# Kernel tuning notes

Measured on AMD Instinct MI355X. Metric: run time of the kernel, lower is better.

The kernel has to match this reference:

```python
import jax, jax.numpy as jnp
import numpy as np
from jax import lax

EPS = 1e-6  # LayerNorm2d eps


def _ln2d(x, w, b):
    # channel-wise LayerNorm over dim 1 of [B,C,H,W]
    mu = jnp.mean(x, axis=1, keepdims=True)
    var = jnp.mean((x - mu) ** 2, axis=1, keepdims=True)
    return (x - mu) / jnp.sqrt(var + EPS) * w[None, :, None, None] + b[None, :, None, None]


def _conv1x1(x, w, b):
    # w: [O, C]
    return jnp.einsum('bchw,oc->bohw', x, w) + b[None, :, None, None]


def _dconv(x, w, b):
    # 3x3 conv, dilation 4, padding 4 -> same H,W. w: [O, C, 3, 3]
    y = lax.conv_general_dilated(x, w, window_strides=(1, 1),
                                 padding=((4, 4), (4, 4)), rhs_dilation=(4, 4),
                                 dimension_numbers=('NCHW', 'OIHW', 'NCHW'))
    return y + b[None, :, None, None]


def _forward(x_l, x_r, nl_w, nl_b, nr_w, nr_b, lp1_w, lp1_b, rp1_w, rp1_b,
             dl_w, dl_b, dr_w, dr_b, lp2_w, lp2_b, rp2_w, rp2_b, beta, gamma):
    c = x_l.shape[1]
    scale = c ** (-0.5)
    N_l = _ln2d(x_l, nl_w, nl_b)
    N_r = _ln2d(x_r, nr_w, nr_b)
    V_l = jnp.transpose(_conv1x1(x_l, lp2_w, lp2_b), (0, 2, 3, 1))   # [B,H,W,C]
    V_r = jnp.transpose(_conv1x1(x_r, rp2_w, rp2_b), (0, 2, 3, 1))
    Q_l = jnp.transpose(_conv1x1(N_l, lp1_w, lp1_b), (0, 2, 3, 1))   # [B,H,W,C]
    Q_r = jnp.transpose(_conv1x1(N_r, rp1_w, rp1_b), (0, 2, 3, 1))
    K_l_T = jnp.transpose(_dconv(N_l, dl_w, dl_b), (0, 2, 1, 3))     # [B,H,C,W]
    K_r_T = jnp.transpose(_dconv(N_r, dr_w, dr_b), (0, 2, 1, 3))
    # per-row cross attention: [B,H,W,W]
    attn_r2l = jnp.einsum('bhwc,bhcv->bhwv', Q_l, K_r_T) * scale
    attn_l2r = jnp.einsum('bhwc,bhcv->bhwv', Q_r, K_l_T) * scale
    F_r2l = jnp.einsum('bhwv,bhvc->bhwc', jax.nn.softmax(attn_r2l, axis=-1), V_r)
    F_l2r = jnp.einsum('bhwv,bhvc->bhwc', jax.nn.softmax(attn_l2r, axis=-1), V_l)
    F_r2l = jnp.transpose(F_r2l, (0, 3, 1, 2)) * beta   # [B,C,H,W]
    F_l2r = jnp.transpose(F_l2r, (0, 3, 1, 2)) * gamma
    return x_l + F_r2l, x_r + F_l2r


def setup_inputs() -> dict:
    key = jax.random.key(0)
    ks = jax.random.split(key, 12)
    B, C, H, W = 2, 128, 192, 512
    s = 0.02
    rn = lambda k, shp: s * jax.random.normal(k, shp, jnp.float32)
    return {
        'x_l': jax.random.normal(ks[0], (B, C, H, W), jnp.float32),
        'x_r': jax.random.normal(ks[1], (B, C, H, W), jnp.float32),
        'nl_w': jnp.ones((C,), jnp.float32), 'nl_b': jnp.zeros((C,), jnp.float32),
        'nr_w': jnp.ones((C,), jnp.float32), 'nr_b': jnp.zeros((C,), jnp.float32),
        'lp1_w': rn(ks[2], (C, C)), 'lp1_b': jnp.zeros((C,), jnp.float32),
        'rp1_w': rn(ks[3], (C, C)), 'rp1_b': jnp.zeros((C,), jnp.float32),
        'dl_w': rn(ks[4], (C, C, 3, 3)), 'dl_b': jnp.zeros((C,), jnp.float32),
        'dr_w': rn(ks[5], (C, C, 3, 3)), 'dr_b': jnp.zeros((C,), jnp.float32),
        'lp2_w': rn(ks[6], (C, C)), 'lp2_b': jnp.zeros((C,), jnp.float32),
        'rp2_w': rn(ks[7], (C, C)), 'rp2_b': jnp.zeros((C,), jnp.float32),
        'beta': 0.1 * jax.random.normal(ks[8], (1, C, 1, 1), jnp.float32),
        'gamma': 0.1 * jax.random.normal(ks[9], (1, C, 1, 1), jnp.float32),
    }


def reference(x_l, x_r, nl_w, nl_b, nr_w, nr_b, lp1_w, lp1_b, rp1_w, rp1_b,
              dl_w, dl_b, dr_w, dr_b, lp2_w, lp2_b, rp2_w, rp2_b, beta, gamma):
    return _forward(x_l, x_r, nl_w, nl_b, nr_w, nr_b, lp1_w, lp1_b, rp1_w, rp1_b,
                    dl_w, dl_b, dr_w, dr_b, lp2_w, lp2_b, rp2_w, rp2_b, beta, gamma)
```

## Files before the change

kernel.cpp:

```cpp
#include <hip/hip_runtime.h>
#include <stdint.h>

#define CC 128
#define HH 192
#define WW 512
#define BB 2
#define HW (HH*WW)
#define CHW (CC*HW)
#define TENS (BB*CHW)

typedef __attribute__((ext_vector_type(8))) short bf16x8;
typedef __attribute__((ext_vector_type(4))) float f32x4;
typedef __attribute__((ext_vector_type(4))) unsigned short u16x4;

__device__ __forceinline__ unsigned short f2bf(float f) {
    union { float f; unsigned u; } v; v.f = f;
    return (unsigned short)((v.u + 0x7FFFu + ((v.u >> 16) & 1u)) >> 16);
}
__device__ __forceinline__ float bf2f(unsigned short u) {
    union { unsigned u; float f; } v; v.u = ((unsigned)u) << 16;
    return v.f;
}
__device__ __forceinline__ uint32_t cvtpk(float lo, float hi) {
    uint32_t r;
    asm("v_cvt_pk_bf16_f32 %0, %1, %2" : "=v"(r) : "v"(lo), "v"(hi));
    return r;
}
__device__ __forceinline__ f32x4 MFMA(bf16x8 a, bf16x8 b, f32x4 c) {
    return __builtin_amdgcn_mfma_f32_16x16x32_bf16(a, b, c, 0, 0, 0);
}

__global__ __launch_bounds__(256) void wcast_k(
    const float* __restrict__ dlw, const float* __restrict__ drw,
    unsigned short* __restrict__ wd)
{
    int i = blockIdx.x * 256 + threadIdx.x;
    if (i >= 2 * 9 * CC * CC) return;
    int e  = i & 7;
    int l  = (i >> 3) & 63;
    int n_ = (i >> 9) & 3;
    int kk = (i >> 11) & 3;
    int oh = (i >> 13) & 1;
    int rest = i >> 14;
    int tap = rest % 9;
    int side = rest / 9;
    int o = oh * 64 + n_ * 16 + (l & 15);
    int c = kk * 32 + (l >> 4) * 8 + e;
    const float* src = side ? drw : dlw;
    wd[i] = f2bf(src[((size_t)o * CC + c) * 9 + tap]);
}

__global__ __launch_bounds__(256) void lnv_k(
    const float* __restrict__ xl, const float* __restrict__ xr,
    const float* __restrict__ nlw, const float* __restrict__ nlb,
    const float* __restrict__ nrw, const float* __restrict__ nrb,
    const float* __restrict__ wlp, const float* __restrict__ blp,
    const float* __restrict__ wrp, const float* __restrict__ brp,
    unsigned short* __restrict__ ntl, unsigned short* __restrict__ ntr,
    unsigned short* __restrict__ vlo, unsigned short* __restrict__ vro)
{
    const int side = blockIdx.y;
    const float* x  = side ? xr : xl;
    const float* nw = side ? nrw : nlw;
    const float* nb = side ? nrb : nlb;
    const float* wv = side ? wrp : wlp;
    const float* bv = side ? brp : blp;
    unsigned short* nt = side ? ntr : ntl;
    unsigned short* vo = side ? vro : vlo;
    const int bid = blockIdx.x;
    const int wt = bid & 7, h = (bid >> 3) % HH, b = bid / (8 * HH);
    const int w0 = wt * 64;
    const int t = threadIdx.x;

    __shared__ unsigned short sA[64][136];
    __shared__ unsigned short sB[128][136];
    __shared__ float red[8][64];
    __shared__ float smu[64], srs[64];

    {
        const int w = t & 63, cg = t >> 6;
        const float* xp = x + (size_t)b * CHW + (size_t)h * WW + w0 + w;
        float s = 0.f, q = 0.f;
        for (int i = 0; i < 16; i++) {
            int c = cg * 32 + i * 2;
            float v0 = xp[(size_t)c * HW];
            float v1 = xp[(size_t)(c + 1) * HW];
            *(uint32_t*)&sA[w][c] = cvtpk(v0, v1);
            s += v0 + v1; q += v0 * v0 + v1 * v1;
        }
        red[cg][w] = s; red[4 + cg][w] = q;
    }
    for (int it = 0; it < 16; it++) {
        int f = it * 1024 + t * 4;
        int o = f >> 7, c = f & 127;
        float4 v = *(const float4*)(wv + o * CC + c);
        *(uint32_t*)&sB[o][c]     = cvtpk(v.x, v.y);
        *(uint32_t*)&sB[o][c + 2] = cvtpk(v.z, v.w);
    }
    __syncthreads();
    if (t < 64) {
        float S = red[0][t] + red[1][t] + red[2][t] + red[3][t];
        float Q = red[4][t] + red[5][t] + red[6][t] + red[7][t];
        float mu = S * (1.f / CC);
        float var = fmaxf(Q * (1.f / CC) - mu * mu, 0.f);
        smu[t] = mu; srs[t] = rsqrtf(var + 1e-6f);
    }
    __syncthreads();
    {
        const int w = t >> 2, c0 = (t & 3) * 32;
        const float mu = smu[w], rs = srs[w];
        unsigned short* np = nt + ((size_t)(b * HH + h) * WW + w0 + w) * CC;
        for (int i = 0; i < 32; i += 2) {
            int c = c0 + i;
            float v0 = (bf2f(sA[w][c]) - mu) * rs * nw[c] + nb[c];
            float v1 = (bf2f(sA[w][c + 1]) - mu) * rs * nw[c + 1] + nb[c + 1];
            *(uint32_t*)&np[c] = cvtpk(v0, v1);
        }
    }
    const int wid = t >> 6, l = t & 63, lr = l & 15, lg = l >> 4;
    f32x4 acc[8] = {};
    for (int kk = 0; kk < 4; kk++) {
        bf16x8 a = *(const bf16x8*)&sA[wid * 16 + lr][kk * 32 + lg * 8];
#pragma unroll
        for (int n_ = 0; n_ < 8; n_++) {
            bf16x8 bb = *(const bf16x8*)&sB[n_ * 16 + lr][kk * 32 + lg * 8];
            acc[n_] = MFMA(a, bb, acc[n_]);
        }
    }
    unsigned short* vp = vo + ((size_t)(b * HH + h) * CC) * WW + w0;
    for (int n_ = 0; n_ < 8; n_++) {
        int o = n_ * 16 + lr;
        float bias = bv[o];
        uint2 uu;
        uu.x = cvtpk(acc[n_][0] + bias, acc[n_][1] + bias);
        uu.y = cvtpk(acc[n_][2] + bias, acc[n_][3] + bias);
        *(uint2*)&vp[(size_t)o * WW + wid * 16 + lg * 4] = uu;
    }
}

__global__ __launch_bounds__(256) void dconv_k(
    const unsigned short* __restrict__ ntl, const unsigned short* __restrict__ ntr,
    const unsigned short* __restrict__ wfr,
    const float* __restrict__ dlb, const float* __restrict__ drb,
    unsigned short* __restrict__ klo, unsigned short* __restrict__ kro)
{
    const int side = blockIdx.y;
    const unsigned short* nt = side ? ntr : ntl;
    const unsigned short* wbase = wfr + (size_t)side * 9 * 16384;
    const float* bd = side ? drb : dlb;
    unsigned short* ko = side ? kro : klo;
    const int bid0 = blockIdx.x;
    const int lgc = (bid0 & 7) * 192 + (bid0 >> 3);
    const int wt = lgc & 3;
    const int hb = lgc >> 2;
    const int h = hb % HH, b = hb / HH;
    const int w0 = wt * 128;
    const int t = threadIdx.x;
    const int wid = t >> 6, l = t & 63, lr = l & 15, lg = l >> 4;
    const int whalf = wid & 1, ohalf = wid >> 1;

    __shared__ unsigned short sA[136][136];

    f32x4 acc[4][4] = {};
    for (int dy = 0; dy < 3; dy++) {
        const int hh = h + 4 * (dy - 1);
        const bool hok = (hh >= 0 && hh < HH);
        __syncthreads();
        for (int f = t * 8; f < 136 * 128; f += 2048) {
            int wloc = f >> 7, c = f & 127;
            int w = w0 - 4 + wloc;
            bf16x8 v = {0, 0, 0, 0, 0, 0, 0, 0};
            if (hok && w >= 0 && w < WW)
                v = *(const bf16x8*)(nt + ((size_t)(b * HH + hh) * WW + w) * CC + c);
            *(bf16x8*)&sA[wloc][c] = v;
        }
        __syncthreads();
#pragma unroll
        for (int dx = 0; dx < 3; dx++) {
            const unsigned short* wtap =
                wbase + (size_t)(dy * 3 + dx) * 16384 + ohalf * 8192 + l * 8;
#pragma unroll
            for (int kk = 0; kk < 4; kk++) {
                bf16x8 bfr[4];
#pragma unroll
                for (int n_ = 0; n_ < 4; n_++)
                    bfr[n_] = *(const bf16x8*)(wtap + (kk * 4 + n_) * 512);
                bf16x8 af[4];
#pragma unroll
                for (int g = 0; g < 4; g++)
                    af[g] = *(const bf16x8*)&sA[whalf * 64 + g * 16 + lr + 4 * dx][kk * 32 + lg * 8];
#pragma unroll
                for (int g = 0; g < 4; g++)
#pragma unroll
                    for (int n_ = 0; n_ < 4; n_++)
                        acc[g][n_] = MFMA(af[g], bfr[n_], acc[g][n_]);
            }
        }
    }
    unsigned short* kp = ko + ((size_t)(b * HH + h) * WW + w0) * CC;
    for (int g = 0; g < 4; g++)
        for (int n_ = 0; n_ < 4; n_++) {
            int o = ohalf * 64 + n_ * 16 + lr;
            float bias = bd[o];
            for (int j = 0; j < 4; j++) {
                int w = whalf * 64 + g * 16 + lg * 4 + j;
                kp[(size_t)w * CC + o] = f2bf(acc[g][n_][j] + bias);
            }
        }
}

__global__ __launch_bounds__(256, 2) void attn_k(
    const unsigned short* __restrict__ ntl, const unsigned short* __restrict__ ntr,
    const unsigned short* __restrict__ kl,  const unsigned short* __restrict__ kr,
    const unsigned short* __restrict__ vtl, const unsigned short* __restrict__ vtr,
    const float* __restrict__ lp1w, const float* __restrict__ lp1b,
    const float* __restrict__ rp1w, const float* __restrict__ rp1b,
    const float* __restrict__ xl, const float* __restrict__ xr,
    const float* __restrict__ beta, const float* __restrict__ gamma,
    float* __restrict__ out)
{
    __shared__ __align__(16) char smem[52224];
    unsigned short* sQ  = (unsigned short*)smem;
    unsigned short* sWh = (unsigned short*)(smem + 34816);
    unsigned short* sKt = (unsigned short*)smem;
    unsigned short* sVt = (unsigned short*)(smem + 17408);

    const int dir = blockIdx.z;
    const unsigned short* nq  = dir ? ntr : ntl;
    const unsigned short* kws = dir ? kl : kr;
    const unsigned short* vws = dir ? vtl : vtr;
    const float* wq   = dir ? rp1w : lp1w;
    const float* bq   = dir ? rp1b : lp1b;
    const float* xres = dir ? xr : xl;
    const float* mult = dir ? gamma : beta;
    float* op = out + (size_t)dir * TENS;

    const int bid = blockIdx.x;
    const int xcd = bid & 7;
    const int s   = bid >> 3;
    const int qb  = s & 3;
    const int bh  = xcd + 8 * (s >> 2);
    const int q0  = qb * 128;
    const int t = threadIdx.x;
    const int wid = t >> 6, l = t & 63, lr = l & 15, lg = l >> 4;

    const unsigned short* ksrc = kws + (size_t)bh * WW * CC;
    const unsigned short* vsrc = vws + (size_t)bh * CC * WW;

    bf16x8 kreg[4], vreg[4];
#pragma unroll
    for (int it = 0; it < 4; it++) {
        int f = it * 2048 + t * 8;
        kreg[it] = *(const bf16x8*)(ksrc + f);
    }
#pragma unroll
    for (int it = 0; it < 4; it++) {
        int f = it * 2048 + t * 8;
        int c = f >> 6, k = f & 63;
        vreg[it] = *(const bf16x8*)(vsrc + (size_t)c * WW + k);
    }

    {
        const unsigned short* nsrc = nq + ((size_t)bh * WW + q0) * CC;
        for (int it = 0; it < 8; it++) {
            int f = it * 2048 + t * 8;
            *(bf16x8*)&sQ[(f >> 7) * 136 + (f & 127)] = *(const bf16x8*)(nsrc + f);
        }
        for (int it = 0; it < 8; it++) {
            int f = it * 1024 + t * 4;
            int o = f >> 7, c = f & 127;
            float4 v = *(const float4*)(wq + o * CC + c);
            *(uint32_t*)&sWh[o * 136 + c]     = cvtpk(v.x, v.y);
            *(uint32_t*)&sWh[o * 136 + c + 2] = cvtpk(v.z, v.w);
        }
    }
    f32x4 qacc[2][8] = {};
    __syncthreads();
    for (int kk = 0; kk < 4; kk++) {
        bf16x8 a0 = *(const bf16x8*)&sQ[(wid * 32 + lr) * 136 + kk * 32 + lg * 8];
        bf16x8 a1 = *(const bf16x8*)&sQ[(wid * 32 + 16 + lr) * 136 + kk * 32 + lg * 8];
#pragma unroll
        for (int n_ = 0; n_ < 4; n_++) {
            bf16x8 b = *(const bf16x8*)&sWh[(n_ * 16 + lr) * 136 + kk * 32 + lg * 8];
            qacc[0][n_] = MFMA(a0, b, qacc[0][n_]);
            qacc[1][n_] = MFMA(a1, b, qacc[1][n_]);
        }
    }
    __syncthreads();
    for (int it = 0; it < 8; it++) {
        int f = it * 1024 + t * 4;
        int o = f >> 7, c = f & 127;
        float4 v = *(const float4*)(wq + (o + 64) * CC + c);
        *(uint32_t*)&sWh[o * 136 + c]     = cvtpk(v.x, v.y);
        *(uint32_t*)&sWh[o * 136 + c + 2] = cvtpk(v.z, v.w);
    }
    __syncthreads();
    for (int kk = 0; kk < 4; kk++) {
        bf16x8 a0 = *(const bf16x8*)&sQ[(wid * 32 + lr) * 136 + kk * 32 + lg * 8];
        bf16x8 a1 = *(const bf16x8*)&sQ[(wid * 32 + 16 + lr) * 136 + kk * 32 + lg * 8];
#pragma unroll
        for (int n_ = 0; n_ < 4; n_++) {
            bf16x8 b = *(const bf16x8*)&sWh[(n_ * 16 + lr) * 136 + kk * 32 + lg * 8];
            qacc[0][4 + n_] = MFMA(a0, b, qacc[0][4 + n_]);
            qacc[1][4 + n_] = MFMA(a1, b, qacc[1][4 + n_]);
        }
    }
    __syncthreads();
    {
        const float SCL = 0.08838834764831845f * 1.4426950408889634f;
#pragma unroll
        for (int mg = 0; mg < 2; mg++)
#pragma unroll
            for (int n_ = 0; n_ < 8; n_++) {
                float bias = bq[n_ * 16 + lr];
#pragma unroll
                for (int j = 0; j < 4; j++)
                    sQ[(wid * 32 + mg * 16 + lg * 4 + j) * 136 + n_ * 16 + lr] =
                        f2bf((qacc[mg][n_][j] + bias) * SCL);
            }
    }
    __syncthreads();
    bf16x8 qf[2][4];
#pragma unroll
    for (int qg = 0; qg < 2; qg++)
#pragma unroll
        for (int kk = 0; kk < 4; kk++)
            qf[qg][kk] = *(const bf16x8*)&sQ[(wid * 32 + qg * 16 + lr) * 136 + kk * 32 + lg * 8];

    f32x4 oacc[8][2] = {};
    float mrow[2] = {-1e30f, -1e30f};
    float lrow[2] = {0.f, 0.f};
    const int src0 = lr + ((l & 16) << 1);
    const int src1 = src0 + 16;
    const int hi = lg >> 1;

    for (int kb = 0; kb < 8; kb++) {
        __syncthreads();
#pragma unroll
        for (int it = 0; it < 4; it++) {
            int f = it * 2048 + t * 8;
            *(bf16x8*)&sKt[(f >> 7) * 136 + (f & 127)] = kreg[it];
        }
#pragma unroll
        for (int it = 0; it < 4; it++) {
            int f = it * 2048 + t * 8;
            int c = f >> 6, k = f & 63;
            *(bf16x8*)&sVt[c * 72 + k] = vreg[it];
        }
        if (kb < 7) {
#pragma unroll
            for (int it = 0; it < 4; it++) {
                int f = it * 2048 + t * 8;
                kreg[it] = *(const bf16x8*)(ksrc + (kb + 1) * 64 * CC + f);
            }
#pragma unroll
            for (int it = 0; it < 4; it++) {
                int f = it * 2048 + t * 8;
                int c = f >> 6, k = f & 63;
                vreg[it] = *(const bf16x8*)(vsrc + (size_t)c * WW + (kb + 1) * 64 + k);
            }
        }
        __syncthreads();
        f32x4 sacc[2][4] = {};
        __builtin_amdgcn_s_setprio(1);
        for (int kk = 0; kk < 4; kk++)
#pragma unroll
            for (int n_ = 0; n_ < 4; n_++) {
                bf16x8 kf = *(const bf16x8*)&sKt[(n_ * 16 + lr) * 136 + kk * 32 + lg * 8];
                sacc[0][n_] = MFMA(kf, qf[0][kk], sacc[0][n_]);
                sacc[1][n_] = MFMA(kf, qf[1][kk], sacc[1][n_]);
            }
        __builtin_amdgcn_s_setprio(0);
        float pm[2];
#pragma unroll
        for (int qg = 0; qg < 2; qg++) {
            float m_ = sacc[qg][0][0];
#pragma unroll
            for (int n_ = 0; n_ < 4; n_++)
#pragma unroll
                for (int j = 0; j < 4; j++) m_ = fmaxf(m_, sacc[qg][n_][j]);
            m_ = fmaxf(m_, __shfl_xor(m_, 16, 64));
            m_ = fmaxf(m_, __shfl_xor(m_, 32, 64));
            pm[qg] = m_;
        }
        bool need = (pm[0] - mrow[0] > 8.f) || (pm[1] - mrow[1] > 8.f);
        if (__any(need)) {
            float al[2];
#pragma unroll
            for (int qg = 0; qg < 2; qg++) {
                float mn = fmaxf(mrow[qg], pm[qg]);
                al[qg] = exp2f(mrow[qg] - mn);
                mrow[qg] = mn;
                lrow[qg] *= al[qg];
            }
#pragma unroll
            for (int n_ = 0; n_ < 8; n_++)
#pragma unroll
                for (int qg = 0; qg < 2; qg++) {
                    f32x4 o = oacc[n_][qg];
                    o[0] *= al[qg]; o[1] *= al[qg]; o[2] *= al[qg]; o[3] *= al[qg];
                    oacc[n_][qg] = o;
                }
        }
#pragma unroll
        for (int qg = 0; qg < 2; qg++) {
            float rs = 0.f;
#pragma unroll
            for (int n_ = 0; n_ < 4; n_++)
#pragma unroll
                for (int j = 0; j < 4; j++) {
                    float e = exp2f(sacc[qg][n_][j] - mrow[qg]);
                    sacc[qg][n_][j] = e;
                    rs += e;
                }
            rs += __shfl_xor(rs, 16, 64);
            rs += __shfl_xor(rs, 32, 64);
            lrow[qg] += rs;
        }
        uint32_t pk[2][4][2];
#pragma unroll
        for (int qg = 0; qg < 2; qg++)
#pragma unroll
            for (int n_ = 0; n_ < 4; n_++) {
                pk[qg][n_][0] = cvtpk(sacc[qg][n_][0], sacc[qg][n_][1]);
                pk[qg][n_][1] = cvtpk(sacc[qg][n_][2], sacc[qg][n_][3]);
            }
#pragma unroll
        for (int kk = 0; kk < 2; kk++) {
            union { uint32_t u[4]; bf16x8 v; } pf[2];
#pragma unroll
            for (int qg = 0; qg < 2; qg++) {
                uint32_t q00 = __shfl(pk[qg][kk * 2][0],     src0, 64);
                uint32_t q01 = __shfl(pk[qg][kk * 2][1],     src0, 64);
                uint32_t q02 = __shfl(pk[qg][kk * 2][0],     src1, 64);
                uint32_t q03 = __shfl(pk[qg][kk * 2][1],     src1, 64);
                uint32_t q10 = __shfl(pk[qg][kk * 2 + 1][0], src0, 64);
                uint32_t q11 = __shfl(pk[qg][kk * 2 + 1][1], src0, 64);
                uint32_t q12 = __shfl(pk[qg][kk * 2 + 1][0], src1, 64);
                uint32_t q13 = __shfl(pk[qg][kk * 2 + 1][1], src1, 64);
                pf[qg].u[0] = hi ? q10 : q00;
                pf[qg].u[1] = hi ? q11 : q01;
                pf[qg].u[2] = hi ? q12 : q02;
                pf[qg].u[3] = hi ? q13 : q03;
            }
            __builtin_amdgcn_s_setprio(1);
#pragma unroll
            for (int n_ = 0; n_ < 8; n_++) {
                bf16x8 va = *(const bf16x8*)&sVt[(n_ * 16 + lr) * 72 + kk * 32 + lg * 8];
                oacc[n_][0] = MFMA(va, pf[0].v, oacc[n_][0]);
                oacc[n_][1] = MFMA(va, pf[1].v, oacc[n_][1]);
            }
            __builtin_amdgcn_s_setprio(0);
        }
    }

    const float inv0 = 1.f / lrow[0], inv1 = 1.f / lrow[1];
    const int b = bh / HH, h = bh % HH;
    const int w_0 = q0 + wid * 32 + lr;
    const float* xp0 = xres + (size_t)b * CHW + (size_t)h * WW + w_0;
    float* outp0 = op + (size_t)b * CHW + (size_t)h * WW + w_0;
#pragma unroll
    for (int n_ = 0; n_ < 8; n_++) {
        float4 m4 = *(const float4*)&mult[n_ * 16 + lg * 4];
#pragma unroll
        for (int j = 0; j < 4; j++) {
            int c = n_ * 16 + lg * 4 + j;
            float mj = (&m4.x)[j];
            outp0[(size_t)c * HW]      = xp0[(size_t)c * HW]      + oacc[n_][0][j] * inv0 * mj;
            outp0[(size_t)c * HW + 16] = xp0[(size_t)c * HW + 16] + oacc[n_][1][j] * inv1 * mj;
        }
    }
}

extern "C" void kernel_launch(void* const* d_in, const int* in_sizes, int n_in,
                              void* d_out, int out_size, void* d_ws, size_t ws_size,
                              hipStream_t stream)
{
    const float* xl   = (const float*)d_in[0];
    const float* xr   = (const float*)d_in[1];
    const float* nlw  = (const float*)d_in[2];
    const float* nlb  = (const float*)d_in[3];
    const float* nrw  = (const float*)d_in[4];
    const float* nrb  = (const float*)d_in[5];
    const float* lp1w = (const float*)d_in[6];
    const float* lp1b = (const float*)d_in[7];
    const float* rp1w = (const float*)d_in[8];
    const float* rp1b = (const float*)d_in[9];
    const float* dlw  = (const float*)d_in[10];
    const float* dlb  = (const float*)d_in[11];
    const float* drw  = (const float*)d_in[12];
    const float* drb  = (const float*)d_in[13];
    const float* lp2w = (const float*)d_in[14];
    const float* lp2b = (const float*)d_in[15];
    const float* rp2w = (const float*)d_in[16];
    const float* rp2b = (const float*)d_in[17];
    const float* beta = (const float*)d_in[18];
    const float* gamma= (const float*)d_in[19];
    float* out = (float*)d_out;

    unsigned short* ws = (unsigned short*)d_ws;
    const size_t A = (size_t)TENS;
    unsigned short* Ntl = ws;
    unsigned short* Ntr = ws + A;
    unsigned short* Kl  = ws + 2 * A;
    unsigned short* Kr  = ws + 3 * A;
    unsigned short* Vtl = ws + 4 * A;
    unsigned short* Vtr = ws + 5 * A;
    unsigned short* Wd  = ws + 6 * A;

    wcast_k<<<dim3(1152), 256, 0, stream>>>(dlw, drw, Wd);
    lnv_k<<<dim3(3072, 2), 256, 0, stream>>>(xl, xr, nlw, nlb, nrw, nrb,
        lp2w, lp2b, rp2w, rp2b, Ntl, Ntr, Vtl, Vtr);
    dconv_k<<<dim3(1536, 2), 256, 0, stream>>>(Ntl, Ntr, Wd, dlb, drb, Kl, Kr);
    attn_k<<<dim3(1536, 1, 2), 256, 0, stream>>>(Ntl, Ntr, Kl, Kr, Vtl, Vtr,
        lp1w, lp1b, rp1w, rp1b, xl, xr, beta, gamma, out);
}
```

Baseline: 543.0 us.

## Feed P directly to 16x16x16 MFMA instead of shuffling to K=32 layout

In the attention P·V stage, the softmax probabilities are now packed straight from the score accumulator layout into bf16x4 operands and consumed by 16x16x16 bf16 MFMA. This removes the cross-lane shuffles and selects that previously rearranged P into the 16x16x32 operand layout. The cost is twice as many MFMA instructions with half the K each, plus narrower LDS reads of V. Separately, the LayerNorm write-out is remapped so each thread handles a fixed channel pair across 16 rows, which should make the global stores coalesced and hoist the weight/bias loads out of the loop.

```diff
diff --git a/kernel.cpp b/kernel.cpp
--- a/kernel.cpp
+++ b/kernel.cpp
@@ -10,8 +10,8 @@
 #define TENS (BB*CHW)
 
 typedef __attribute__((ext_vector_type(8))) short bf16x8;
+typedef __attribute__((ext_vector_type(4))) short bf16x4;
 typedef __attribute__((ext_vector_type(4))) float f32x4;
-typedef __attribute__((ext_vector_type(4))) unsigned short u16x4;
 
 __device__ __forceinline__ unsigned short f2bf(float f) {
     union { float f; unsigned u; } v; v.f = f;
@@ -28,6 +28,17 @@
 }
 __device__ __forceinline__ f32x4 MFMA(bf16x8 a, bf16x8 b, f32x4 c) {
     return __builtin_amdgcn_mfma_f32_16x16x32_bf16(a, b, c, 0, 0, 0);
+}
+__device__ __forceinline__ f32x4 MFMA16(bf16x4 a, bf16x4 b, f32x4 c) {
+#if __has_builtin(__builtin_amdgcn_mfma_f32_16x16x16_bf16)
+    return __builtin_amdgcn_mfma_f32_16x16x16_bf16(a, b, c, 0, 0, 0);
+#elif __has_builtin(__builtin_amdgcn_mfma_f32_16x16x16bf16_1k)
+    return __builtin_amdgcn_mfma_f32_16x16x16bf16_1k(a, b, c, 0, 0, 0);
+#else
+    f32x4 d = c;
+    asm("v_mfma_f32_16x16x16_bf16 %0, %1, %2, %0" : "+v"(d) : "v"(a), "v"(b));
+    return d;
+#endif
 }
 
 __global__ __launch_bounds__(256) void wcast_k(
@@ -107,14 +118,16 @@
     }
     __syncthreads();
     {
-        const int w = t >> 2, c0 = (t & 3) * 32;
-        const float mu = smu[w], rs = srs[w];
-        unsigned short* np = nt + ((size_t)(b * HH + h) * WW + w0 + w) * CC;
-        for (int i = 0; i < 32; i += 2) {
-            int c = c0 + i;
-            float v0 = (bf2f(sA[w][c]) - mu) * rs * nw[c] + nb[c];
-            float v1 = (bf2f(sA[w][c + 1]) - mu) * rs * nw[c + 1] + nb[c + 1];
-            *(uint32_t*)&np[c] = cvtpk(v0, v1);
+        const int cl = (t & 63) * 2, wg = t >> 6;
+        const float nwa = nw[cl], nwb = nw[cl + 1];
+        const float nba = nb[cl], nbb = nb[cl + 1];
+        unsigned short* npb = nt + ((size_t)(b * HH + h) * WW + w0) * CC;
+        for (int wp = 0; wp < 16; wp++) {
+            int w = wp * 4 + wg;
+            float mu = smu[w], rs = srs[w];
+            float v0 = (bf2f(sA[w][cl]) - mu) * rs * nwa + nba;
+            float v1 = (bf2f(sA[w][cl + 1]) - mu) * rs * nwb + nbb;
+            *(uint32_t*)&npb[(size_t)w * CC + cl] = cvtpk(v0, v1);
         }
     }
     const int wid = t >> 6, l = t & 63, lr = l & 15, lg = l >> 4;
@@ -330,9 +343,6 @@
     f32x4 oacc[8][2] = {};
     float mrow[2] = {-1e30f, -1e30f};
     float lrow[2] = {0.f, 0.f};
-    const int src0 = lr + ((l & 16) << 1);
-    const int src1 = src0 + 16;
-    const int hi = lg >> 1;
 
     for (int kb = 0; kb < 8; kb++) {
         __syncthreads();
@@ -417,41 +427,22 @@
             rs += __shfl_xor(rs, 32, 64);
             lrow[qg] += rs;
         }
-        uint32_t pk[2][4][2];
-#pragma unroll
-        for (int qg = 0; qg < 2; qg++)
-#pragma unroll
-            for (int n_ = 0; n_ < 4; n_++) {
-                pk[qg][n_][0] = cvtpk(sacc[qg][n_][0], sacc[qg][n_][1]);
-                pk[qg][n_][1] = cvtpk(sacc[qg][n_][2], sacc[qg][n_][3]);
-            }
-#pragma unroll
-        for (int kk = 0; kk < 2; kk++) {
-            union { uint32_t u[4]; bf16x8 v; } pf[2];
-#pragma unroll
-            for (int qg = 0; qg < 2; qg++) {
-                uint32_t q00 = __shfl(pk[qg][kk * 2][0],     src0, 64);
-                uint32_t q01 = __shfl(pk[qg][kk * 2][1],     src0, 64);
-                uint32_t q02 = __shfl(pk[qg][kk * 2][0],     src1, 64);
-                uint32_t q03 = __shfl(pk[qg][kk * 2][1],     src1, 64);
-                uint32_t q10 = __shfl(pk[qg][kk * 2 + 1][0], src0, 64);
-                uint32_t q11 = __shfl(pk[qg][kk * 2 + 1][1], src0, 64);
-                uint32_t q12 = __shfl(pk[qg][kk * 2 + 1][0], src1, 64);
-                uint32_t q13 = __shfl(pk[qg][kk * 2 + 1][1], src1, 64);
-                pf[qg].u[0] = hi ? q10 : q00;
-                pf[qg].u[1] = hi ? q11 : q01;
-                pf[qg].u[2] = hi ? q12 : q02;
-                pf[qg].u[3] = hi ? q13 : q03;
-            }
-            __builtin_amdgcn_s_setprio(1);
-#pragma unroll
-            for (int n_ = 0; n_ < 8; n_++) {
-                bf16x8 va = *(const bf16x8*)&sVt[(n_ * 16 + lr) * 72 + kk * 32 + lg * 8];
-                oacc[n_][0] = MFMA(va, pf[0].v, oacc[n_][0]);
-                oacc[n_][1] = MFMA(va, pf[1].v, oacc[n_][1]);
-            }
-            __builtin_amdgcn_s_setprio(0);
-        }
+        __builtin_amdgcn_s_setprio(1);
+#pragma unroll
+        for (int n_ = 0; n_ < 4; n_++) {
+            union { uint32_t u[2]; bf16x4 v; } b0, b1;
+            b0.u[0] = cvtpk(sacc[0][n_][0], sacc[0][n_][1]);
+            b0.u[1] = cvtpk(sacc[0][n_][2], sacc[0][n_][3]);
+            b1.u[0] = cvtpk(sacc[1][n_][0], sacc[1][n_][1]);
+            b1.u[1] = cvtpk(sacc[1][n_][2], sacc[1][n_][3]);
+#pragma unroll
+            for (int n8 = 0; n8 < 8; n8++) {
+                bf16x4 va = *(const bf16x4*)&sVt[(n8 * 16 + lr) * 72 + n_ * 16 + lg * 4];
+                oacc[n8][0] = MFMA16(va, b0.v, oacc[n8][0]);
+                oacc[n8][1] = MFMA16(va, b1.v, oacc[n8][1]);
+            }
+        }
+        __builtin_amdgcn_s_setprio(0);
     }
 
     const float inv0 = 1.f / lrow[0], inv1 = 1.f / lrow[1];
```

Result: faster. 505.7 us (-6.9%).
